# Kernel tuning notes

Measured on AMD Instinct MI355X. Metric: run time of the kernel, lower is better.

Reference implementation:

```python
import jax, jax.numpy as jnp
import numpy as np
import math

B, S, D, H = 4, 2048, 512, 8
HD = D // H  # head dim = 64

def setup_inputs() -> dict:
    key = jax.random.key(0)
    ks = jax.random.split(key, 12)
    inp = {
        'queries': jax.random.normal(ks[0], (B, S, D), jnp.float32),
        'keys': jax.random.normal(ks[1], (B, S, D), jnp.float32),
        'values': jax.random.normal(ks[2], (B, S, D), jnp.float32),
        'valid_lens': jax.random.randint(ks[3], (B,), 0, 2048, jnp.int32),
        'Wq': jax.random.normal(ks[4], (D, D), jnp.float32) / math.sqrt(D),
        'bq': jnp.zeros((D,), jnp.float32),
        'Wk': jax.random.normal(ks[5], (D, D), jnp.float32) / math.sqrt(D),
        'bk': jnp.zeros((D,), jnp.float32),
        'Wv': jax.random.normal(ks[6], (D, D), jnp.float32) / math.sqrt(D),
        'bv': jnp.zeros((D,), jnp.float32),
        'Wo': jax.random.normal(ks[7], (D, D), jnp.float32) / math.sqrt(D),
        'bo': jnp.zeros((D,), jnp.float32),
    }
    return inp

def reference(queries, keys, values, valid_lens, Wq, bq, Wk, bk, Wv, bv, Wo, bo):
    # project and split heads: [B,S,D] -> [B,H,S,HD]
    def split_heads(x):
        return x.reshape(B, S, H, HD).transpose(0, 2, 1, 3)
    q = split_heads(queries @ Wq + bq)
    k = split_heads(keys @ Wk + bk)
    v = split_heads(values @ Wv + bv)
    # scores [B,H,Sq,Sk]
    scores = jnp.einsum('bhqd,bhkd->bhqk', q, k) / math.sqrt(HD)
    # masked softmax: mask key positions >= valid_len with -1e6 (d2l semantics)
    mask = jnp.arange(S)[None, None, None, :] < valid_lens[:, None, None, None]
    scores = jnp.where(mask, scores, -1e6)
    attn = jax.nn.softmax(scores, axis=-1)
    out = jnp.einsum('bhqk,bhkd->bhqd', attn, v)  # [B,H,S,HD]
    out = out.transpose(0, 2, 1, 3).reshape(B, S, D)
    return out @ Wo + bo
```

## Files before the change

### kernel.cpp

```cpp
#include <hip/hip_runtime.h>
#include <hip/hip_bf16.h>

typedef _Float16 half8 __attribute__((ext_vector_type(8)));
typedef _Float16 half4 __attribute__((ext_vector_type(4)));
typedef float floatx4 __attribute__((ext_vector_type(4)));

#define LOG2E 1.44269504088896340736f

__device__ __forceinline__ half8 cvt8r(floatx4 a, floatx4 b) {
    half8 h;
    h[0] = (_Float16)a[0]; h[1] = (_Float16)a[1]; h[2] = (_Float16)a[2]; h[3] = (_Float16)a[3];
    h[4] = (_Float16)b[0]; h[5] = (_Float16)b[1]; h[6] = (_Float16)b[2]; h[7] = (_Float16)b[3];
    return h;
}

__global__ __launch_bounds__(256) void transpose_w_kernel(
        const float* __restrict__ Wq, const float* __restrict__ Wk,
        const float* __restrict__ Wv, const float* __restrict__ Wo,
        _Float16* __restrict__ out) {
    const float* W = (blockIdx.z == 0) ? Wq : (blockIdx.z == 1) ? Wk : (blockIdx.z == 2) ? Wv : Wo;
    _Float16* o = out + (size_t)blockIdx.z * 512 * 512;
    __shared__ __align__(16) _Float16 t[64][72];
    int r0 = blockIdx.x * 64, c0 = blockIdx.y * 64;
    int tid = threadIdx.x;
    for (int i = 0; i < 2; i++) {
        int f = i * 256 + tid;
        int row = f >> 3, seg = f & 7;
        const float* p = W + (size_t)(r0 + row) * 512 + c0 + seg * 8;
        *(half8*)&t[row][seg * 8] = cvt8r(*(const floatx4*)p, *(const floatx4*)(p + 4));
    }
    __syncthreads();
    for (int i = 0; i < 2; i++) {
        int f = i * 256 + tid;
        int crow = f >> 3, seg = f & 7;
        half8 hv;
        for (int j = 0; j < 8; j++) hv[j] = t[seg * 8 + j][crow];
        *(half8*)(o + (size_t)(c0 + crow) * 512 + r0 + seg * 8) = hv;
    }
}

__global__ __launch_bounds__(256) void gemm_qkv_kernel(
        const float* __restrict__ Xq, const float* __restrict__ Xk, const float* __restrict__ Xv,
        const _Float16* __restrict__ WTall,
        const float* __restrict__ bq, const float* __restrict__ bk, const float* __restrict__ bv,
        const int* __restrict__ vlens,
        _Float16* __restrict__ qo, _Float16* __restrict__ ko2, _Float16* __restrict__ vto) {
    int z = blockIdx.z;
    int mBase = blockIdx.x * 64, nBase = blockIdx.y * 128;

    if (z >= 1) {
        int b_ = mBase >> 11, s0 = mBase & 2047;
        int L = vlens[b_];
        if (s0 >= L && !(z == 2 && L == 0)) return;
    }

    const float* X = (z == 0) ? Xq : (z == 1) ? Xk : Xv;
    const _Float16* BT = WTall + (size_t)z * 512 * 512;
    const float* bias = (z == 0) ? bq : (z == 1) ? bk : bv;

    __shared__ __align__(16) _Float16 Asm[64][72];
    __shared__ __align__(16) _Float16 Bsm[128][72];

    int tid = threadIdx.x;
    int wave = tid >> 6, lane = tid & 63;
    int lrow = lane & 15, quad = lane >> 4;
    int mrow = wave * 16 + lrow;

    const floatx4 fz = {0.f, 0.f, 0.f, 0.f};
    floatx4 acc[8];
    for (int i = 0; i < 8; i++) acc[i] = fz;

    int arow[2], aseg[2], brow[4], bseg[4];
    for (int i = 0; i < 2; i++) { int f = i * 256 + tid; arow[i] = f >> 3; aseg[i] = f & 7; }
    for (int i = 0; i < 4; i++) { int f = i * 256 + tid; brow[i] = f >> 3; bseg[i] = f & 7; }

    floatx4 areg[2][2];
    half8 breg[4];
    for (int i = 0; i < 2; i++) {
        const float* pa = X + (size_t)(mBase + arow[i]) * 512 + aseg[i] * 8;
        areg[i][0] = *(const floatx4*)pa;
        areg[i][1] = *(const floatx4*)(pa + 4);
    }
    for (int i = 0; i < 4; i++)
        breg[i] = *(const half8*)(BT + (size_t)(nBase + brow[i]) * 512 + bseg[i] * 8);

    for (int kb = 0; kb < 512; kb += 64) {
        for (int i = 0; i < 2; i++) *(half8*)&Asm[arow[i]][aseg[i] * 8] = cvt8r(areg[i][0], areg[i][1]);
        for (int i = 0; i < 4; i++) *(half8*)&Bsm[brow[i]][bseg[i] * 8] = breg[i];
        __syncthreads();
        if (kb + 64 < 512) {
            int kn = kb + 64;
            for (int i = 0; i < 2; i++) {
                const float* pa = X + (size_t)(mBase + arow[i]) * 512 + kn + aseg[i] * 8;
                areg[i][0] = *(const floatx4*)pa;
                areg[i][1] = *(const floatx4*)(pa + 4);
            }
            for (int i = 0; i < 4; i++)
                breg[i] = *(const half8*)(BT + (size_t)(nBase + brow[i]) * 512 + kn + bseg[i] * 8);
        }
        for (int kc = 0; kc < 2; kc++) {
            int ko_ = kc * 32 + quad * 8;
            half8 a = *(const half8*)&Asm[mrow][ko_];
            for (int nt = 0; nt < 8; nt++) {
                half8 b = *(const half8*)&Bsm[nt * 16 + lrow][ko_];
                acc[nt] = __builtin_amdgcn_mfma_f32_16x16x32_f16(a, b, acc[nt], 0, 0, 0);
            }
        }
        __syncthreads();
    }

    if (z == 2) {
        for (int nt = 0; nt < 8; nt++) {
            int gc = nBase + nt * 16 + lrow;
            float bb = bias[gc];
            int h = gc >> 6, hd = gc & 63;
            int gr = mBase + wave * 16 + quad * 4;
            int b_ = gr >> 11, s = gr & 2047;
            half4 hv;
            for (int r = 0; r < 4; r++) hv[r] = (_Float16)(acc[nt][r] + bb);
            *(half4*)(vto + (((size_t)(b_ * 8 + h) * 64 + hd) * 2048 + s)) = hv;
        }
    } else {
        _Float16* out = (z == 0) ? qo : ko2;
        for (int nt = 0; nt < 8; nt++) {
            int gc = nBase + nt * 16 + lrow;
            float bb = bias[gc];
            int h = gc >> 6, hd = gc & 63;
            for (int r = 0; r < 4; r++) {
                int gr = mBase + wave * 16 + quad * 4 + r;
                int b_ = gr >> 11, s = gr & 2047;
                out[(((size_t)b_ * 8 + h) * 2048 + s) * 64 + hd] = (_Float16)(acc[nt][r] + bb);
            }
        }
    }
}

__global__ __launch_bounds__(128) void attn_kernel(
        const _Float16* __restrict__ qws, const _Float16* __restrict__ kws, const _Float16* __restrict__ vtws,
        const int* __restrict__ vlens, _Float16* __restrict__ aout) {
    int idx = blockIdx.x;
    int b = ((idx & 3) + (idx >> 8)) & 3;
    int h = (idx >> 2) & 7;
    int q0 = ((idx >> 5) & 63) * 32;
    int bh = b * 8 + h;
    int L = vlens[b];
    bool uni = (L == 0);
    int nkt = uni ? 32 : ((L + 63) >> 6);
    int nfull = uni ? 0 : (L >> 6);

    int tid = threadIdx.x;
    int w = tid >> 6, lane = tid & 63;
    int lrow = lane & 15, quad = lane >> 4;

    __shared__ __align__(16) _Float16 ksm[64][72];
    __shared__ __align__(16) _Float16 vtsm[64][72];

    const _Float16* qbase = qws + ((size_t)bh * 2048 + q0) * 64;
    const _Float16* kbase = kws + (size_t)bh * 2048 * 64;
    const _Float16* vtbase = vtws + (size_t)bh * 64 * 2048;

    half8 qf[2];
    for (int kc = 0; kc < 2; kc++) {
        qf[kc] = *(const half8*)(qbase + (w * 16 + lrow) * 64 + kc * 32 + quad * 8);
        qf[kc] = qf[kc] * (_Float16)(0.125f * LOG2E);
    }

    half4 onesf;
    {
        _Float16 o1 = (lrow == 0) ? (_Float16)1.0f : (_Float16)0.0f;
        onesf[0] = o1; onesf[1] = o1; onesf[2] = o1; onesf[3] = o1;
    }

    const floatx4 fz = {0.f, 0.f, 0.f, 0.f};
    floatx4 oacc[5];
    for (int nt = 0; nt < 5; nt++) oacc[nt] = fz;

    int srow[4], sseg[4];
    for (int i = 0; i < 4; i++) { int f = i * 128 + tid; srow[i] = f >> 3; sseg[i] = f & 7; }
    half8 kreg[4], vreg[4];
    for (int i = 0; i < 4; i++) {
        kreg[i] = *(const half8*)(kbase + (i * 128 + tid) * 8);
        vreg[i] = *(const half8*)(vtbase + (size_t)srow[i] * 2048 + sseg[i] * 8);
    }

    for (int kt = 0; kt < nkt; kt++) {
        for (int i = 0; i < 4; i++) {
            *(half8*)&ksm[srow[i]][sseg[i] * 8]  = kreg[i];
            *(half8*)&vtsm[srow[i]][sseg[i] * 8] = vreg[i];
        }
        __syncthreads();
        if (kt + 1 < nkt) {
            const _Float16* ktn = kbase + (size_t)(kt + 1) * 4096;
            const _Float16* vtn = vtbase + (kt + 1) * 64;
            for (int i = 0; i < 4; i++) {
                kreg[i] = *(const half8*)(ktn + (i * 128 + tid) * 8);
                vreg[i] = *(const half8*)(vtn + (size_t)srow[i] * 2048 + sseg[i] * 8);
            }
        }

        floatx4 sacc[4];
        for (int km = 0; km < 4; km++) sacc[km] = fz;
        for (int kc = 0; kc < 2; kc++) {
            int ko_ = kc * 32 + quad * 8;
            for (int km = 0; km < 4; km++) {
                half8 kf = *(const half8*)&ksm[km * 16 + lrow][ko_];
                sacc[km] = __builtin_amdgcn_mfma_f32_16x16x32_f16(kf, qf[kc], sacc[km], 0, 0, 0);
            }
        }

        half4 pf[4];
        if (kt < nfull) {
            for (int km = 0; km < 4; km++)
                for (int r = 0; r < 4; r++)
                    pf[km][r] = (_Float16)exp2f(sacc[km][r]);
        } else {
            int kb0 = kt * 64 + quad * 4;
            for (int km = 0; km < 4; km++) {
                int kb = kb0 + km * 16;
                for (int r = 0; r < 4; r++) {
                    float p = uni ? 1.0f : ((kb + r < L) ? exp2f(sacc[km][r]) : 0.0f);
                    pf[km][r] = (_Float16)p;
                }
            }
        }

        for (int km = 0; km < 4; km++) {
            int kk = km * 16 + quad * 4;
            for (int nt = 0; nt < 4; nt++) {
                half4 bvf = *(const half4*)&vtsm[nt * 16 + lrow][kk];
                oacc[nt] = __builtin_amdgcn_mfma_f32_16x16x16f16(pf[km], bvf, oacc[nt], 0, 0, 0);
            }
            oacc[4] = __builtin_amdgcn_mfma_f32_16x16x16f16(pf[km], onesf, oacc[4], 0, 0, 0);
        }
        __syncthreads();
    }

    float inv[4];
    for (int r = 0; r < 4; r++)
        inv[r] = 1.0f / __shfl(oacc[4][r], quad << 4, 64);

    for (int nt = 0; nt < 4; nt++) {
        for (int r = 0; r < 4; r++) {
            int s = q0 + w * 16 + quad * 4 + r;
            aout[((size_t)b * 2048 + s) * 512 + h * 64 + nt * 16 + lrow] =
                (_Float16)(oacc[nt][r] * inv[r]);
        }
    }
}

__global__ __launch_bounds__(256) void gemm_out_kernel(
        const _Float16* __restrict__ A, const _Float16* __restrict__ BT,
        const float* __restrict__ bias, float* __restrict__ out) {
    __shared__ __align__(16) _Float16 Asm[64][72];
    __shared__ __align__(16) _Float16 Bsm[128][72];

    int tid = threadIdx.x;
    int wave = tid >> 6, lane = tid & 63;
    int lrow = lane & 15, quad = lane >> 4;
    int mBase = blockIdx.x * 64, nBase = blockIdx.y * 128;
    int mrow = wave * 16 + lrow;

    const floatx4 fz = {0.f, 0.f, 0.f, 0.f};
    floatx4 acc[8];
    for (int i = 0; i < 8; i++) acc[i] = fz;

    int arow[2], aseg[2], brow[4], bseg[4];
    for (int i = 0; i < 2; i++) { int f = i * 256 + tid; arow[i] = f >> 3; aseg[i] = f & 7; }
    for (int i = 0; i < 4; i++) { int f = i * 256 + tid; brow[i] = f >> 3; bseg[i] = f & 7; }

    half8 areg[2], breg[4];
    for (int i = 0; i < 2; i++)
        areg[i] = *(const half8*)(A + (size_t)(mBase + arow[i]) * 512 + aseg[i] * 8);
    for (int i = 0; i < 4; i++)
        breg[i] = *(const half8*)(BT + (size_t)(nBase + brow[i]) * 512 + bseg[i] * 8);

    for (int kb = 0; kb < 512; kb += 64) {
        for (int i = 0; i < 2; i++) *(half8*)&Asm[arow[i]][aseg[i] * 8] = areg[i];
        for (int i = 0; i < 4; i++) *(half8*)&Bsm[brow[i]][bseg[i] * 8] = breg[i];
        __syncthreads();
        if (kb + 64 < 512) {
            int kn = kb + 64;
            for (int i = 0; i < 2; i++)
                areg[i] = *(const half8*)(A + (size_t)(mBase + arow[i]) * 512 + kn + aseg[i] * 8);
            for (int i = 0; i < 4; i++)
                breg[i] = *(const half8*)(BT + (size_t)(nBase + brow[i]) * 512 + kn + bseg[i] * 8);
        }
        for (int kc = 0; kc < 2; kc++) {
            int ko_ = kc * 32 + quad * 8;
            half8 a = *(const half8*)&Asm[mrow][ko_];
            for (int nt = 0; nt < 8; nt++) {
                half8 b = *(const half8*)&Bsm[nt * 16 + lrow][ko_];
                acc[nt] = __builtin_amdgcn_mfma_f32_16x16x32_f16(a, b, acc[nt], 0, 0, 0);
            }
        }
        __syncthreads();
    }

    for (int nt = 0; nt < 8; nt++) {
        int gc = nBase + nt * 16 + lrow;
        float bb = bias[gc];
        for (int r = 0; r < 4; r++) {
            int gr = mBase + wave * 16 + quad * 4 + r;
            out[(size_t)gr * 512 + gc] = acc[nt][r] + bb;
        }
    }
}

extern "C" void kernel_launch(void* const* d_in, const int* in_sizes, int n_in,
                              void* d_out, int out_size, void* d_ws, size_t ws_size,
                              hipStream_t stream) {
    const float* Q  = (const float*)d_in[0];
    const float* K  = (const float*)d_in[1];
    const float* V  = (const float*)d_in[2];
    const int*   VL = (const int*)d_in[3];
    const float* Wq = (const float*)d_in[4];
    const float* bq = (const float*)d_in[5];
    const float* Wk = (const float*)d_in[6];
    const float* bk = (const float*)d_in[7];
    const float* Wv = (const float*)d_in[8];
    const float* bv = (const float*)d_in[9];
    const float* Wo = (const float*)d_in[10];
    const float* bo = (const float*)d_in[11];

    char* ws = (char*)d_ws;
    _Float16* WT   = (_Float16*)ws;
    _Float16* qws  = (_Float16*)(ws + (size_t)(2)  * 1024 * 1024);
    _Float16* kws  = (_Float16*)(ws + (size_t)(10) * 1024 * 1024);
    _Float16* aout = (_Float16*)(ws + (size_t)(18) * 1024 * 1024);
    _Float16* vtws = (_Float16*)(ws + (size_t)(26) * 1024 * 1024);

    transpose_w_kernel<<<dim3(8, 8, 4), 256, 0, stream>>>(Wq, Wk, Wv, Wo, WT);
    gemm_qkv_kernel<<<dim3(128, 4, 3), 256, 0, stream>>>(Q, K, V, WT, bq, bk, bv, VL, qws, kws, vtws);
    attn_kernel<<<dim3(2048, 1, 1), 128, 0, stream>>>(qws, kws, vtws, VL, aout);
    gemm_out_kernel<<<dim3(128, 4, 1), 256, 0, stream>>>(aout, WT + (size_t)3 * 512 * 512, bo, (float*)d_out);
}
```

Before: 192.8 us.

## Rewrite attention with 32x32x16 MFMA, 64-query blocks, and XOR-swizzled LDS

The attention kernel now assigns 64 queries per block (32 per wave) and uses 32x32x16 f16 MFMAs for both QK^T and PV, halving the grid. This doubles K/V tile reuse per LDS load. The padded shared arrays are replaced by XOR-swizzled layouts to avoid bank conflicts. The row sum is accumulated in registers instead of through an extra ones-MFMA. In exchange, register pressure rises and the number of blocks drops, which may reduce occupancy.

New measurement: 194.0 us. About the same (+0.6%).

```diff
diff --git a/kernel.cpp b/kernel.cpp
--- a/kernel.cpp
+++ b/kernel.cpp
@@ -4,6 +4,8 @@
 typedef _Float16 half8 __attribute__((ext_vector_type(8)));
 typedef _Float16 half4 __attribute__((ext_vector_type(4)));
 typedef float floatx4 __attribute__((ext_vector_type(4)));
+typedef float floatx16 __attribute__((ext_vector_type(16)));
+typedef unsigned int uint2v __attribute__((ext_vector_type(2)));
 
 #define LOG2E 1.44269504088896340736f
 
@@ -13,6 +15,8 @@
     h[4] = (_Float16)b[0]; h[5] = (_Float16)b[1]; h[6] = (_Float16)b[2]; h[7] = (_Float16)b[3];
     return h;
 }
+
+union H8U { half8 h; uint2v u[2]; };
 
 __global__ __launch_bounds__(256) void transpose_w_kernel(
         const float* __restrict__ Wq, const float* __restrict__ Wk,
@@ -136,12 +140,13 @@
 }
 
 __global__ __launch_bounds__(128) void attn_kernel(
-        const _Float16* __restrict__ qws, const _Float16* __restrict__ kws, const _Float16* __restrict__ vtws,
-        const int* __restrict__ vlens, _Float16* __restrict__ aout) {
+        const _Float16* __restrict__ qws, const _Float16* __restrict__ kws,
+        const _Float16* __restrict__ vtws, const int* __restrict__ vlens,
+        _Float16* __restrict__ aout) {
     int idx = blockIdx.x;
     int b = ((idx & 3) + (idx >> 8)) & 3;
     int h = (idx >> 2) & 7;
-    int q0 = ((idx >> 5) & 63) * 32;
+    int q0 = ((idx >> 5) & 31) * 64;
     int bh = b * 8 + h;
     int L = vlens[b];
     bool uni = (L == 0);
@@ -149,102 +154,133 @@
     int nfull = uni ? 0 : (L >> 6);
 
     int tid = threadIdx.x;
-    int w = tid >> 6, lane = tid & 63;
-    int lrow = lane & 15, quad = lane >> 4;
-
-    __shared__ __align__(16) _Float16 ksm[64][72];
-    __shared__ __align__(16) _Float16 vtsm[64][72];
-
-    const _Float16* qbase = qws + ((size_t)bh * 2048 + q0) * 64;
+    int wq = tid >> 6;
+    int lane = tid & 63;
+    int l31 = lane & 31, hi = lane >> 5;
+
+    __shared__ __align__(16) _Float16 ksm[64 * 64];
+    __shared__ __align__(16) _Float16 vtsm[64 * 64];
+    char* ksmB = (char*)ksm;
+    char* vsmB = (char*)vtsm;
+
     const _Float16* kbase = kws + (size_t)bh * 2048 * 64;
     const _Float16* vtbase = vtws + (size_t)bh * 64 * 2048;
 
-    half8 qf[2];
-    for (int kc = 0; kc < 2; kc++) {
-        qf[kc] = *(const half8*)(qbase + (w * 16 + lrow) * 64 + kc * 32 + quad * 8);
-        qf[kc] = qf[kc] * (_Float16)(0.125f * LOG2E);
-    }
-
-    half4 onesf;
+    half8 qf[4];
     {
-        _Float16 o1 = (lrow == 0) ? (_Float16)1.0f : (_Float16)0.0f;
-        onesf[0] = o1; onesf[1] = o1; onesf[2] = o1; onesf[3] = o1;
-    }
-
-    const floatx4 fz = {0.f, 0.f, 0.f, 0.f};
-    floatx4 oacc[5];
-    for (int nt = 0; nt < 5; nt++) oacc[nt] = fz;
-
-    int srow[4], sseg[4];
-    for (int i = 0; i < 4; i++) { int f = i * 128 + tid; srow[i] = f >> 3; sseg[i] = f & 7; }
+        const _Float16* qrow = qws + ((size_t)bh * 2048 + q0 + wq * 32 + l31) * 64;
+#pragma unroll
+        for (int kc = 0; kc < 4; kc++) {
+            qf[kc] = *(const half8*)(qrow + kc * 16 + hi * 8);
+            qf[kc] = qf[kc] * (_Float16)(0.125f * LOG2E);
+        }
+    }
+
+    floatx16 oacc0, oacc1;
+#pragma unroll
+    for (int i = 0; i < 16; i++) { oacc0[i] = 0.f; oacc1[i] = 0.f; }
+    float rs = 0.f;
+
+    int seg = tid & 7;
+    int trow = tid >> 3;
+    int xr = (l31 & 15) << 3;
+
     half8 kreg[4], vreg[4];
+#pragma unroll
     for (int i = 0; i < 4; i++) {
-        kreg[i] = *(const half8*)(kbase + (i * 128 + tid) * 8);
-        vreg[i] = *(const half8*)(vtbase + (size_t)srow[i] * 2048 + sseg[i] * 8);
+        int row = i * 16 + trow;
+        kreg[i] = *(const half8*)(kbase + row * 64 + seg * 8);
+        vreg[i] = *(const half8*)(vtbase + (size_t)row * 2048 + seg * 8);
     }
 
     for (int kt = 0; kt < nkt; kt++) {
+#pragma unroll
         for (int i = 0; i < 4; i++) {
-            *(half8*)&ksm[srow[i]][sseg[i] * 8]  = kreg[i];
-            *(half8*)&vtsm[srow[i]][sseg[i] * 8] = vreg[i];
+            int row = i * 16 + trow;
+            int wo = row * 128 + ((seg * 16) ^ ((row & 15) << 3));
+            H8U kv, vv;
+            kv.h = kreg[i]; vv.h = vreg[i];
+            *(uint2v*)(ksmB + wo) = kv.u[0];
+            *(uint2v*)(ksmB + (wo ^ 8)) = kv.u[1];
+            *(uint2v*)(vsmB + wo) = vv.u[0];
+            *(uint2v*)(vsmB + (wo ^ 8)) = vv.u[1];
         }
         __syncthreads();
         if (kt + 1 < nkt) {
-            const _Float16* ktn = kbase + (size_t)(kt + 1) * 4096;
-            const _Float16* vtn = vtbase + (kt + 1) * 64;
+            const _Float16* kn = kbase + (size_t)(kt + 1) * 4096;
+            const _Float16* vn = vtbase + (kt + 1) * 64;
+#pragma unroll
             for (int i = 0; i < 4; i++) {
-                kreg[i] = *(const half8*)(ktn + (i * 128 + tid) * 8);
-                vreg[i] = *(const half8*)(vtn + (size_t)srow[i] * 2048 + sseg[i] * 8);
-            }
-        }
-
-        floatx4 sacc[4];
-        for (int km = 0; km < 4; km++) sacc[km] = fz;
-        for (int kc = 0; kc < 2; kc++) {
-            int ko_ = kc * 32 + quad * 8;
-            for (int km = 0; km < 4; km++) {
-                half8 kf = *(const half8*)&ksm[km * 16 + lrow][ko_];
-                sacc[km] = __builtin_amdgcn_mfma_f32_16x16x32_f16(kf, qf[kc], sacc[km], 0, 0, 0);
-            }
-        }
-
-        half4 pf[4];
-        if (kt < nfull) {
-            for (int km = 0; km < 4; km++)
-                for (int r = 0; r < 4; r++)
-                    pf[km][r] = (_Float16)exp2f(sacc[km][r]);
-        } else {
-            int kb0 = kt * 64 + quad * 4;
-            for (int km = 0; km < 4; km++) {
-                int kb = kb0 + km * 16;
-                for (int r = 0; r < 4; r++) {
-                    float p = uni ? 1.0f : ((kb + r < L) ? exp2f(sacc[km][r]) : 0.0f);
-                    pf[km][r] = (_Float16)p;
+                int row = i * 16 + trow;
+                kreg[i] = *(const half8*)(kn + row * 64 + seg * 8);
+                vreg[i] = *(const half8*)(vn + (size_t)row * 2048 + seg * 8);
+            }
+        }
+
+#pragma unroll
+        for (int t = 0; t < 2; t++) {
+            floatx16 sacc;
+#pragma unroll
+            for (int i = 0; i < 16; i++) sacc[i] = 0.f;
+            int rbase = (t * 32 + l31) * 128;
+#pragma unroll
+            for (int kc = 0; kc < 4; kc++) {
+                int off = rbase + ((kc * 32 + hi * 16) ^ xr);
+                H8U kf;
+                kf.u[0] = *(const uint2v*)(ksmB + off);
+                kf.u[1] = *(const uint2v*)(ksmB + (off ^ 8));
+                sacc = __builtin_amdgcn_mfma_f32_32x32x16_f16(kf.h, qf[kc], sacc, 0, 0, 0);
+            }
+
+            float p[16];
+            if (kt < nfull) {
+#pragma unroll
+                for (int r = 0; r < 16; r++) p[r] = exp2f(sacc[r]);
+            } else {
+                int kb0 = kt * 64 + t * 32 + 4 * hi;
+#pragma unroll
+                for (int r = 0; r < 16; r++) {
+                    int key = kb0 + (r & 3) + 8 * (r >> 2);
+                    p[r] = uni ? 1.0f : ((key < L) ? exp2f(sacc[r]) : 0.0f);
                 }
             }
-        }
-
-        for (int km = 0; km < 4; km++) {
-            int kk = km * 16 + quad * 4;
-            for (int nt = 0; nt < 4; nt++) {
-                half4 bvf = *(const half4*)&vtsm[nt * 16 + lrow][kk];
-                oacc[nt] = __builtin_amdgcn_mfma_f32_16x16x16f16(pf[km], bvf, oacc[nt], 0, 0, 0);
-            }
-            oacc[4] = __builtin_amdgcn_mfma_f32_16x16x16f16(pf[km], onesf, oacc[4], 0, 0, 0);
-        }
-        __syncthreads();
-    }
-
-    float inv[4];
-    for (int r = 0; r < 4; r++)
-        inv[r] = 1.0f / __shfl(oacc[4][r], quad << 4, 64);
-
-    for (int nt = 0; nt < 4; nt++) {
-        for (int r = 0; r < 4; r++) {
-            int s = q0 + w * 16 + quad * 4 + r;
-            aout[((size_t)b * 2048 + s) * 512 + h * 64 + nt * 16 + lrow] =
-                (_Float16)(oacc[nt][r] * inv[r]);
-        }
+#pragma unroll
+            for (int r = 0; r < 16; r++) rs += p[r];
+
+#pragma unroll
+            for (int s2 = 0; s2 < 2; s2++) {
+                int s = t * 2 + s2;
+                H8U pa;
+#pragma unroll
+                for (int j = 0; j < 8; j++) pa.h[j] = (_Float16)p[s2 * 8 + j];
+                int cb = (s * 32 + hi * 8) ^ xr;
+                {
+                    int off = l31 * 128 + cb;
+                    H8U vf;
+                    vf.u[0] = *(const uint2v*)(vsmB + off);
+                    vf.u[1] = *(const uint2v*)(vsmB + (off ^ 16));
+                    oacc0 = __builtin_amdgcn_mfma_f32_32x32x16_f16(pa.h, vf.h, oacc0, 0, 0, 0);
+                }
+                {
+                    int off = (32 + l31) * 128 + cb;
+                    H8U vf;
+                    vf.u[0] = *(const uint2v*)(vsmB + off);
+                    vf.u[1] = *(const uint2v*)(vsmB + (off ^ 16));
+                    oacc1 = __builtin_amdgcn_mfma_f32_32x32x16_f16(pa.h, vf.h, oacc1, 0, 0, 0);
+                }
+            }
+        }
+        __syncthreads();
+    }
+
+    float rstot = rs + __shfl_xor(rs, 32, 64);
+    _Float16* outb = aout + ((size_t)b * 2048 + q0 + wq * 32) * 512 + h * 64;
+#pragma unroll
+    for (int r = 0; r < 16; r++) {
+        int qi = (r & 3) + 8 * (r >> 2) + 4 * hi;
+        float inv = 1.0f / __shfl(rstot, qi, 64);
+        outb[(size_t)qi * 512 + l31] = (_Float16)(oacc0[r] * inv);
+        outb[(size_t)qi * 512 + 32 + l31] = (_Float16)(oacc1[r] * inv);
     }
 }
 
@@ -331,6 +367,6 @@
 
     transpose_w_kernel<<<dim3(8, 8, 4), 256, 0, stream>>>(Wq, Wk, Wv, Wo, WT);
     gemm_qkv_kernel<<<dim3(128, 4, 3), 256, 0, stream>>>(Q, K, V, WT, bq, bk, bv, VL, qws, kws, vtws);
-    attn_kernel<<<dim3(2048, 1, 1), 128, 0, stream>>>(qws, kws, vtws, VL, aout);
+    attn_kernel<<<dim3(1024, 1, 1), 128, 0, stream>>>(qws, kws, vtws, VL, aout);
     gemm_out_kernel<<<dim3(128, 4, 1), 256, 0, stream>>>(aout, WT + (size_t)3 * 512 * 512, bo, (float*)d_out);
 }
```
